# Performance work log

Measured on AMD Instinct MI355X. Metric: run time of the kernel, lower is better.

Reference implementation:

```python
import jax, jax.numpy as jnp
import numpy as np
import math
from jax import lax

K = 3  # kernel size for every layer


def _get_size(h, w, stride, ceil_mode):
    ah, aw = h - (K - 1), w - (K - 1)
    if ceil_mode:
        return math.ceil(ah / stride), math.ceil(aw / stride)
    return ah // stride, aw // stride


def _sample(h, w, stride, ceil_mode, mask_out, rng):
    """Replicates SConv2dAvg.sample: random in-stride offsets per output cell,
    plus bottom-up input mask = union of 3x3 windows of selected positions
    where the downstream mask is active."""
    ah, aw = h - (K - 1), w - (K - 1)
    oh, ow = _get_size(h, w, stride, ceil_mode)
    selh = rng.integers(0, stride, (oh, ow)).astype(np.int32)
    selw = rng.integers(0, stride, (oh, ow)).astype(np.int32)
    resth, restw = oh * stride - ah, ow * stride - aw
    if resth > 0:
        selh[-1, :] = selh[-1, :] % resth
    if restw > 0:
        selw[:, -1] = selw[:, -1] % restw
    ph = selh + (np.arange(oh) * stride)[:, None]  # conv-grid row of selected window
    pw = selw + (np.arange(ow) * stride)[None, :]
    mask_in = np.zeros((h, w), np.int32)
    ys = ph[mask_out == 1]
    xs = pw[mask_out == 1]
    for dy in range(K):
        for dx in range(K):
            mask_in[ys + dy, xs + dx] = 1
    return selh, selw, mask_in


def setup_inputs() -> dict:
    key = jax.random.key(0)
    rng = np.random.default_rng(0)
    B, H0, W0 = 64, 132, 132
    ks = jax.random.split(key, 9)
    x = jax.random.normal(ks[0], (B, 3, H0, W0), jnp.float32)

    def conv_params(kw_, kb_, cout, cin):
        bound = 1.0 / np.sqrt(cin * K * K)
        w = jax.random.uniform(kw_, (cout, cin, K, K), jnp.float32, -bound, bound)
        b = jax.random.uniform(kb_, (cout,), jnp.float32, -bound, bound)
        return w, b

    w1, b1 = conv_params(ks[1], ks[2], 200, 3)
    w2, b2 = conv_params(ks[3], ks[4], 400, 200)
    w3, b3 = conv_params(ks[5], ks[6], 800, 400)
    w4, b4 = conv_params(ks[7], ks[8], 10, 800)

    h1, wd1 = _get_size(H0, W0, 2, False)   # 65,65
    h2, wd2 = _get_size(h1, wd1, 2, False)  # 31,31
    h3, wd3 = _get_size(h2, wd2, 2, True)   # 15,15
    mask3 = np.ones((h3, wd3), np.int32)
    selh3, selw3, mask2 = _sample(h2, wd2, 2, True, mask3, rng)
    selh2, selw2, mask1 = _sample(h1, wd1, 2, False, mask2, rng)
    selh1, selw1, _ = _sample(H0, W0, 2, False, mask1, rng)

    j = jnp.asarray
    return {
        "x": x,
        "w1": w1, "b1": b1, "w2": w2, "b2": b2,
        "w3": w3, "b3": b3, "w4": w4, "b4": b4,
        "selh1": j(selh1), "selw1": j(selw1), "mask1": j(mask1),
        "selh2": j(selh2), "selw2": j(selw2), "mask2": j(mask2),
        "selh3": j(selh3), "selw3": j(selw3), "mask3": j(mask3),
    }


def _sconv_stoch(x, weight, bias, selh, selw, mask, stride):
    """Stochastic strided conv: per output cell, evaluate the 3x3 valid conv at a
    randomly selected position inside its stride x stride block; zero unmasked
    cells (they were never computed), then add bias everywhere."""
    oh, ow = selh.shape
    kh, kw = weight.shape[2], weight.shape[3]
    ph = selh + jnp.arange(oh, dtype=selh.dtype)[:, None] * stride  # (oh,ow)
    pw = selw + jnp.arange(ow, dtype=selw.dtype)[None, :] * stride
    ih = ph[:, :, None, None] + jnp.arange(kh)[None, None, :, None]  # (oh,ow,kh,kw)
    iw = pw[:, :, None, None] + jnp.arange(kw)[None, None, None, :]
    patches = x[:, :, ih, iw]  # (B, Cin, oh, ow, kh, kw)
    out = jnp.einsum('bchwij,ocij->bohw', patches, weight)
    out = jnp.where(mask[None, None] == 1, out, jnp.zeros((), out.dtype))
    return out + bias[None, :, None, None]


def reference(x, w1, b1, w2, b2, w3, b3, w4, b4,
              selh1, selw1, mask1, selh2, selw2, mask2, selh3, selw3, mask3):
    out = jax.nn.relu(_sconv_stoch(x, w1, b1, selh1, selw1, mask1, 2))
    out = jax.nn.relu(_sconv_stoch(out, w2, b2, selh2, selw2, mask2, 2))
    out = jax.nn.relu(_sconv_stoch(out, w3, b3, selh3, selw3, mask3, 2))
    out = lax.conv_general_dilated(out, w4, (1, 1), 'VALID') + b4[None, :, None, None]
    return out.reshape(out.shape[0], -1)
```

## Files before the change

kernel.cpp:

```cpp
#include <hip/hip_runtime.h>
#include <hip/hip_bf16.h>

using bf16 = __hip_bfloat16;
using short8 = __attribute__((ext_vector_type(8))) short;
using sh4 = __attribute__((ext_vector_type(4))) short;
using f32x4 = __attribute__((ext_vector_type(4))) float;

__device__ __align__(16) bf16 g_wp1[16 * 3 * 512];
__device__ __align__(16) bf16 g_wp2[63 * 25 * 512];
__device__ __align__(16) bf16 g_wp3[2 * 117 * 25 * 512];
__device__ __align__(16) bf16 g_wp4[1 * 225 * 512];

__device__ int g_list1[4225];
__device__ int g_list2[961];
__device__ int g_list3[225];
__device__ int g_cnt[3];


__global__ __launch_bounds__(256) void k_pack1(const float* __restrict__ w) {
  int el = blockIdx.x * 256 + threadIdx.x;
  if (el >= 16 * 3 * 512) return;
  int j = el & 7, lane = (el >> 3) & 63, rest = el >> 9;
  int kt = rest % 3, mt = rest / 3;
  int m = mt * 16 + (lane & 15);
  int k = kt * 32 + ((lane >> 4) * 8) + j;
  int chunk = k >> 3, c = k & 7;
  float val = 0.f;
  if (m < 200 && chunk < 9 && c < 3) val = w[((size_t)m * 3 + c) * 9 + chunk];
  g_wp1[el] = __float2bfloat16(val);
}
template <int CIN, int SUBT, int COUT, int KT>
__device__ __forceinline__ void pack_kmaj(const float* __restrict__ w,
                                          bf16* __restrict__ dst, int total) {
  int el = blockIdx.x * 256 + threadIdx.x;
  if (el >= total) return;
  int j = el & 7, lane = (el >> 3) & 63, ti = el >> 9;
  int half = ti / (KT * 25);
  int r2 = ti - half * (KT * 25);
  int kt = r2 / 25, mtl = r2 - kt * 25;
  int mt = half * 25 + mtl;
  int chunk = kt / SUBT, cc = kt - chunk * SUBT;
  int m = mt * 16 + (lane & 15);
  int c = cc * 32 + ((lane >> 4) * 8) + j;
  float val = 0.f;
  if (m < COUT && c < CIN) val = w[((size_t)m * CIN + c) * 9 + chunk];
  dst[el] = __float2bfloat16(val);
}
__global__ __launch_bounds__(256) void k_pack2(const float* __restrict__ w) {
  pack_kmaj<200, 7, 400, 63>(w, g_wp2, 63 * 25 * 512);
}
__global__ __launch_bounds__(256) void k_pack3(const float* __restrict__ w) {
  pack_kmaj<400, 13, 800, 117>(w, g_wp3, 2 * 117 * 25 * 512);
}
__global__ __launch_bounds__(256) void k_pack4(const float* __restrict__ w) {
  int el = blockIdx.x * 256 + threadIdx.x;
  if (el >= 225 * 512) return;
  int j = el & 7, lane = (el >> 3) & 63, rest = el >> 9;
  int kt = rest % 225;
  int chunk = kt / 25, cc = kt - chunk * 25;
  int m = lane & 15;
  int c = cc * 32 + ((lane >> 4) * 8) + j;
  float val = 0.f;
  if (m < 10 && c < 800) val = w[((size_t)m * 800 + c) * 9 + chunk];
  g_wp4[el] = __float2bfloat16(val);
}

__global__ __launch_bounds__(256) void k_compact(const int* __restrict__ m1,
                                                 const int* __restrict__ m2,
                                                 const int* __restrict__ m3) {
  const int which = blockIdx.x;
  const int* m = which == 0 ? m1 : (which == 1 ? m2 : m3);
  int* lst = which == 0 ? g_list1 : (which == 1 ? g_list2 : g_list3);
  const int n = which == 0 ? 4225 : (which == 1 ? 961 : 225);
  const int per = (n + 255) / 256;
  const int lo = threadIdx.x * per;
  const int hi = lo + per < n ? lo + per : n;
  __shared__ int cnt[256];
  __shared__ int off[256];
  int c = 0;
  for (int i = lo; i < hi; ++i) c += (m[i] != 0);
  cnt[threadIdx.x] = c;
  __syncthreads();
  if (threadIdx.x == 0) {
    int s = 0;
    for (int t = 0; t < 256; ++t) { off[t] = s; s += cnt[t]; }
    g_cnt[which] = s;
  }
  __syncthreads();
  int o = off[threadIdx.x];
  for (int i = lo; i < hi; ++i)
    if (m[i] != 0) lst[o++] = i;
}

template <int COUT>
__global__ __launch_bounds__(256) void k_fill_off(const int* __restrict__ mask,
                                                  const float* __restrict__ bias,
                                                  bf16* __restrict__ out_t) {
  constexpr int NFULL = (COUT / 32) * 32;
  constexpr int TW = COUT - NFULL;
  constexpr int TD = TW ? TW * 16 : 1;
  const int pos = blockIdx.x;
  if (mask[pos] != 0) return;
  bf16* base = out_t + (size_t)pos * 64 * COUT;
  for (int idx = threadIdx.x; idx < 64 * COUT / 8; idx += 256) {
    const int e0 = idx * 8;
    int ch0;
    if (e0 < NFULL * 64) {
      const int cc = e0 >> 11;
      const int r = e0 & 2047;
      const int lq = (r >> 7) & 3;
      ch0 = cc * 32 + lq * 8;
    } else {
      const int r = e0 - NFULL * 64;
      const int r2 = r - (r / TD) * TD;
      const int mq = (TW == 16) ? (r2 >> 7) : 0;
      ch0 = NFULL + mq * 8;
    }
    short8 s;
#pragma unroll
    for (int j = 0; j < 8; ++j) {
      float v = bias[ch0 + j];
      v = v > 0.f ? v : 0.f;
      bf16 h = __float2bfloat16(v);
      s[j] = *reinterpret_cast<short*>(&h);
    }
    *reinterpret_cast<short8*>(base + e0) = s;
  }
}

__global__ __launch_bounds__(256) void k_fill_xt(float* __restrict__ p, int n4) {
  int i = blockIdx.x * 256 + threadIdx.x;
  if (i < n4) reinterpret_cast<float4*>(p)[i] = float4{0.f, 0.f, 0.f, 0.f};
}
__global__ __launch_bounds__(256) void k_zero_out(float* __restrict__ p) {
  int i = blockIdx.x * 256 + threadIdx.x;
  if (i < 64 * 10 * 13 * 13) p[i] = 0.f;
}

__global__ __launch_bounds__(256) void k_transpose_x(const float* __restrict__ x,
                                                     bf16* __restrict__ xt) {
  int idx = blockIdx.x * 256 + threadIdx.x;
  constexpr int N = 64 * 3 * 132 * 132;
  if (idx >= N) return;
  int w = idx % 132;
  int t = idx / 132;
  int h = t % 132;
  t /= 132;
  int c = t % 3;
  int b = t / 3;
  xt[((size_t)(h * 132 + w) * 64 + b) * 8 + c] = __float2bfloat16(x[idx]);
}

template <int COUT, int MT>
__device__ __forceinline__ void epilogue_frag(f32x4 (&acc)[MT][4], int pos,
                                              int mt0, int mcnt, int q, int nl,
                                              const float* bias, bf16* out_t) {
  constexpr int NFULL = (COUT / 32) * 32;
  constexpr int TW = COUT - NFULL;
  bf16* cell = out_t + (size_t)pos * (COUT * 64);
#pragma unroll
  for (int ms = 0; ms < MT; ++ms) {
    const int T = mt0 + ms;
    const int mbase = T * 16 + q * 4;
    if (ms < mcnt && mbase < COUT) {
      const float4 bv = *reinterpret_cast<const float4*>(bias + mbase);
#pragma unroll
      for (int t = 0; t < 4; ++t) {
        sh4 s;
#pragma unroll
        for (int r = 0; r < 4; ++r) {
          float vv = acc[ms][t][r] + ((const float*)&bv)[r];
          vv = vv > 0.f ? vv : 0.f;
          bf16 h = __float2bfloat16(vv);
          s[r] = *reinterpret_cast<short*>(&h);
        }
        size_t el;
        if (mbase < NFULL) {
          el = ((size_t)((mbase >> 5) * 4 + t) * 64 +
                (((mbase >> 3) & 3) * 16 + nl)) * 8 + (mbase & 7);
        } else {
          el = (size_t)NFULL * 64 + t * (TW * 16) +
               ((TW == 16) ? (((mbase >> 3) & 1) * 128) : 0) + nl * 8 +
               (mbase & 7);
        }
        *reinterpret_cast<sh4*>(cell + el) = s;
      }
    }
  }
}

template <int CINW, int COUT, int WIN, int OW, int KTILES, int MT>
__device__ __forceinline__ void sconv_body_div(
    const bf16* __restrict__ in_t, const bf16* __restrict__ wp,
    const float* __restrict__ bias, const int* __restrict__ selh,
    const int* __restrict__ selw, const int* __restrict__ list, int which,
    bf16* __restrict__ out_t) {
  const int bid = blockIdx.x;
  if (bid >= g_cnt[which]) return;
  const int pos = list[bid];
  const int tid = threadIdx.x;
  const int lane = tid & 63;
  const int wv = tid >> 6;
  const int nl = lane & 15;
  const int q = lane >> 4;
  const int mt0 = blockIdx.y * (4 * MT) + wv * MT;
  f32x4 acc[MT][4] = {};
  const int y = pos / OW, xq = pos % OW;
  const int ph = selh[pos] + 2 * y;
  const int pw = selw[pos] + 2 * xq;
  const short8* ap = reinterpret_cast<const short8*>(wp);
#pragma unroll
  for (int kt = 0; kt < KTILES; ++kt) {
    int k = kt * 32 + q * 8;
    int chunk = (int)((unsigned)k / (unsigned)CINW);
    int c = k - chunk * CINW;
    if (chunk > 8) { chunk = 8; c = 0; }
    const int di = (chunk * 342) >> 10;
    const int dj = chunk - di * 3;
    const bf16* bp =
        in_t + ((size_t)((ph + di) * WIN + (pw + dj)) * 64 + nl) * CINW + c;
    short8 Bf[4];
#pragma unroll
    for (int t = 0; t < 4; ++t)
      Bf[t] = *reinterpret_cast<const short8*>(bp + (size_t)t * 16 * CINW);
    short8 Af[MT];
#pragma unroll
    for (int ms = 0; ms < MT; ++ms)
      Af[ms] = ap[((size_t)(mt0 + ms) * KTILES + kt) * 64 + lane];
#pragma unroll
    for (int ms = 0; ms < MT; ++ms)
#pragma unroll
      for (int t = 0; t < 4; ++t)
        acc[ms][t] =
            __builtin_amdgcn_mfma_f32_16x16x32_bf16(Af[ms], Bf[t], acc[ms][t], 0, 0, 0);
  }
  epilogue_frag<COUT, MT>(acc, pos, mt0, MT, q, nl, bias, out_t);
}

template <int CIN, int SUBT, int COUT, int WIN, int OW, int NTILE>
__device__ __forceinline__ void sconv_body_pipe(
    const bf16* __restrict__ in_t, const bf16* __restrict__ wp,
    const float* __restrict__ bias, const int* __restrict__ selh,
    const int* __restrict__ selw, const int* __restrict__ list, int which,
    int bid, int myt, bf16* __restrict__ out_t) {
  constexpr int MT = 4;
  constexpr int KTILES = 9 * SUBT;
  constexpr int NFC = CIN / 32;
  constexpr int TIN = CIN - NFC * 32;
  __shared__ __align__(16) bf16 Ab[3][NTILE * 512];
  __shared__ __align__(16) bf16 Bb[3][2 * 2048];
  const int cnt = g_cnt[which];
  if (2 * bid >= cnt) return;
  const int p0 = list[2 * bid];
  const int p1 = list[2 * bid + 1 < cnt ? 2 * bid + 1 : cnt - 1];
  const int tid = threadIdx.x;
  const int lane = tid & 63;
  const int wv = tid >> 6;
  const int g = wv & 7;
  const int pp = wv >> 3;
  const int tstart = (g == 0) ? 0 : 4 + 3 * (g - 1);
  const int tcnt = (g == 0) ? 4 : 3;
  const int stile = (wv < 9) ? wv * 2 : 18 + (wv - 9);
  const int scnt = (wv < 9) ? 2 : 1;
  const int nl = lane & 15;
  const int q = lane >> 4;
  const int y0 = p0 / OW, x0 = p0 % OW;
  const int y1 = p1 / OW, x1 = p1 % OW;
  const int ph0 = selh[p0] + 2 * y0, pw0 = selw[p0] + 2 * x0;
  const int ph1 = selh[p1] + 2 * y1, pw1 = selw[p1] + 2 * x1;

  auto cellp = [&](int ph, int pw, int chunk) -> const bf16* {
    const int di = (chunk * 342) >> 10;
    const int dj = chunk - di * 3;
    return in_t + (size_t)((ph + di) * WIN + (pw + dj)) * (CIN * 64);
  };

  int scc = 0, sch = 0;
  const bf16* scell0 = cellp(ph0, pw0, 0);
  const bf16* scell1 = cellp(ph1, pw1, 0);

  auto stage = [&](int b) {
    const int kt = sch * SUBT + scc;
    const bf16* asrc = wp + ((size_t)kt * NTILE + stile) * 512 + lane * 8;
#pragma unroll
    for (int i = 0; i < 2; ++i) {
      if (i < scnt) {
        __builtin_amdgcn_global_load_lds(
            (const __attribute__((address_space(1))) void*)(asrc + (size_t)i * 512),
            (__attribute__((address_space(3))) void*)(&Ab[b][(stile + i) * 512 +
                                                             lane * 8]),
            16, 0, 0);
      }
    }
    if (wv < 8) {
      const int j = wv & 3;
      const bf16* cell = (wv >> 2) ? scell1 : scell0;
      int boff;
      if (scc < NFC) {
        boff = (scc * 4 + j) * 512;
      } else {
        int jj = (j * 512 < TIN * 64) ? j : 0;
        boff = NFC * 2048 + jj * 512;
      }
      __builtin_amdgcn_global_load_lds(
          (const __attribute__((address_space(1))) void*)(cell + boff + lane * 8),
          (__attribute__((address_space(3))) void*)(&Bb[b][(wv >> 2) * 2048 +
                                                           j * 512 + lane * 8]),
          16, 0, 0);
    }
    if (++scc == SUBT) {
      scc = 0;
      if (++sch > 8) sch = 8;
      scell0 = cellp(ph0, pw0, sch);
      scell1 = cellp(ph1, pw1, sch);
    }
  };

  f32x4 acc[MT][4] = {};

  stage(0);
  stage(1);

  int buf = 0, ccC = 0;
  for (int kt = 0; kt < KTILES; ++kt) {
    __builtin_amdgcn_sched_barrier(0);
    if (kt == KTILES - 1) {
      asm volatile("s_waitcnt vmcnt(0)");
    } else if (wv < 8) {
      asm volatile("s_waitcnt vmcnt(3)");
    } else if (wv == 8) {
      asm volatile("s_waitcnt vmcnt(2)");
    } else {
      asm volatile("s_waitcnt vmcnt(1)");
    }
    __builtin_amdgcn_sched_barrier(0);
    __builtin_amdgcn_s_barrier();
    __builtin_amdgcn_sched_barrier(0);

    short8 Af[MT];
#pragma unroll
    for (int ms = 0; ms < MT; ++ms)
      if (ms < tcnt)
        Af[ms] = *reinterpret_cast<const short8*>(
            &Ab[buf][(tstart + ms) * 512 + lane * 8]);
    short8 Bf[4];
    if (ccC != SUBT - 1) {
#pragma unroll
      for (int t = 0; t < 4; ++t)
        Bf[t] = *reinterpret_cast<const short8*>(
            &Bb[buf][pp * 2048 + t * 512 + lane * 8]);
    } else if (TIN == 8) {
#pragma unroll
      for (int t = 0; t < 4; ++t)
        Bf[t] = *reinterpret_cast<const short8*>(
            &Bb[buf][pp * 2048 + t * 128 + nl * 8]);
    } else {
#pragma unroll
      for (int t = 0; t < 4; ++t)
        Bf[t] = *reinterpret_cast<const short8*>(
            &Bb[buf][pp * 2048 + t * 256 + (q & 1) * 128 + nl * 8]);
    }
    __builtin_amdgcn_s_setprio(1);
#pragma unroll
    for (int ms = 0; ms < MT; ++ms)
      if (ms < tcnt)
#pragma unroll
        for (int t = 0; t < 4; ++t)
          acc[ms][t] = __builtin_amdgcn_mfma_f32_16x16x32_bf16(Af[ms], Bf[t],
                                                               acc[ms][t], 0, 0, 0);
    __builtin_amdgcn_s_setprio(0);
    __builtin_amdgcn_sched_barrier(0);
    if (kt + 2 < KTILES) {
      int sb = buf + 2;
      if (sb >= 3) sb -= 3;
      stage(sb);
    }
    if (++ccC == SUBT) ccC = 0;
    if (++buf == 3) buf = 0;
  }
  const int mt0 = myt * NTILE + tstart;
  epilogue_frag<COUT, MT>(acc, pp ? p1 : p0, mt0, tcnt, q, nl, bias, out_t);
}

__global__ __launch_bounds__(256) void k_sconv1(
    const bf16* __restrict__ in_t, const float* __restrict__ bias,
    const int* __restrict__ selh, const int* __restrict__ selw,
    bf16* __restrict__ out_t) {
  sconv_body_div<8, 200, 132, 65, 3, 4>(in_t, g_wp1, bias, selh, selw, g_list1, 0,
                                        out_t);
}
__global__ __launch_bounds__(1024, 4) void k_sconv2(
    const bf16* __restrict__ in_t, const float* __restrict__ bias,
    const int* __restrict__ selh, const int* __restrict__ selw,
    bf16* __restrict__ out_t) {
  sconv_body_pipe<200, 7, 400, 65, 31, 25>(in_t, g_wp2, bias, selh, selw,
                                           g_list2, 1, blockIdx.x, 0, out_t);
}
__global__ __launch_bounds__(1024, 4) void k_sconv3(
    const bf16* __restrict__ in_t, const float* __restrict__ bias,
    const int* __restrict__ selh, const int* __restrict__ selw,
    bf16* __restrict__ out_t) {
  const int id = blockIdx.x;
  const int xcd = id & 7;
  const int yhalf = xcd >> 2;
  const int slot = (id >> 3) * 4 + (xcd & 3);
  sconv_body_pipe<400, 13, 800, 31, 15, 25>(
      in_t, g_wp3 + (size_t)yhalf * 117 * 25 * 512, bias, selh, selw, g_list3, 2,
      slot, yhalf, out_t);
}

__global__ __launch_bounds__(256) void k_conv4m(
    const bf16* __restrict__ in_t,
    const float* __restrict__ bias,
    float* __restrict__ out) {
  const int pos = blockIdx.x;
  const int y = pos / 13, x = pos % 13;
  const int tid = threadIdx.x;
  const int lane = tid & 63;
  const int wv = tid >> 6;
  const int nl = lane & 15;
  const int q = lane >> 4;
  const int kslice = blockIdx.y * 4 + wv;
  __shared__ f32x4 Racc[4][4][64];
  f32x4 acc[4] = {};
  const short8* ap = reinterpret_cast<const short8*>(g_wp4);
  for (int kt = kslice; kt < 225; kt += 16) {
    const int chunk = kt / 25;
    const int cc = kt - chunk * 25;
    const int di = chunk / 3, dj = chunk - di * 3;
    const bf16* cell = in_t + (size_t)((y + di) * 15 + (x + dj)) * (800 * 64);
    short8 A0 = ap[(size_t)kt * 64 + lane];
    short8 Bf[4];
#pragma unroll
    for (int t = 0; t < 4; ++t)
      Bf[t] = *reinterpret_cast<const short8*>(
          cell + ((size_t)(cc * 4 + t) * 64 + lane) * 8);
#pragma unroll
    for (int t = 0; t < 4; ++t)
      acc[t] = __builtin_amdgcn_mfma_f32_16x16x32_bf16(A0, Bf[t], acc[t], 0, 0, 0);
  }
#pragma unroll
  for (int t = 0; t < 4; ++t) Racc[wv][t][lane] = acc[t];
  __syncthreads();
  if (wv == 0) {
    const int rowb = q * 4;
#pragma unroll
    for (int t = 0; t < 4; ++t) {
      f32x4 s = Racc[0][t][lane];
#pragma unroll
      for (int w2 = 1; w2 < 4; ++w2) {
        f32x4 o = Racc[w2][t][lane];
#pragma unroll
        for (int r = 0; r < 4; ++r) s[r] += o[r];
      }
      const int n = t * 16 + nl;
#pragma unroll
      for (int r = 0; r < 4; ++r) {
        const int m = rowb + r;
        if (m < 10) {
          float v = s[r] + (blockIdx.y == 0 ? bias[m] : 0.f);
          atomicAdd(&out[(((size_t)n * 10 + m) * 13 + y) * 13 + x], v);
        }
      }
    }
  }
}

extern "C" void kernel_launch(void* const* d_in, const int* in_sizes, int n_in,
                              void* d_out, int out_size, void* d_ws, size_t ws_size,
                              hipStream_t stream) {
  const float* x  = (const float*)d_in[0];
  const float* w1 = (const float*)d_in[1];
  const float* b1 = (const float*)d_in[2];
  const float* w2 = (const float*)d_in[3];
  const float* b2 = (const float*)d_in[4];
  const float* w3 = (const float*)d_in[5];
  const float* b3 = (const float*)d_in[6];
  const float* w4 = (const float*)d_in[7];
  const float* b4 = (const float*)d_in[8];
  const int* selh1 = (const int*)d_in[9];
  const int* selw1 = (const int*)d_in[10];
  const int* mask1 = (const int*)d_in[11];
  const int* selh2 = (const int*)d_in[12];
  const int* selw2 = (const int*)d_in[13];
  const int* mask2 = (const int*)d_in[14];
  const int* selh3 = (const int*)d_in[15];
  const int* selw3 = (const int*)d_in[16];
  const int* mask3 = (const int*)d_in[17];

  char* ws = (char*)d_ws;
  bf16* o1t = (bf16*)(ws);
  bf16* xt  = (bf16*)(ws + 108160000);
  bf16* o2t = (bf16*)(ws + 108160000);
  bf16* o3t = (bf16*)(ws);

  k_pack1<<<dim3((16 * 3 * 512 + 255) / 256), dim3(256), 0, stream>>>(w1);
  k_pack2<<<dim3((63 * 25 * 512 + 255) / 256), dim3(256), 0, stream>>>(w2);
  k_pack3<<<dim3((2 * 117 * 25 * 512 + 255) / 256), dim3(256), 0, stream>>>(w3);
  k_pack4<<<dim3((225 * 512 + 255) / 256), dim3(256), 0, stream>>>(w4);
  k_compact<<<dim3(3), dim3(256), 0, stream>>>(mask1, mask2, mask3);
  k_fill_xt<<<dim3((2230272 + 255) / 256), dim3(256), 0, stream>>>((float*)xt, 2230272);
  k_transpose_x<<<dim3((64 * 3 * 132 * 132 + 255) / 256), dim3(256), 0, stream>>>(x, xt);
  k_zero_out<<<dim3((64 * 10 * 13 * 13 + 255) / 256), dim3(256), 0, stream>>>(
      (float*)d_out);

  k_fill_off<200><<<dim3(4225), dim3(256), 0, stream>>>(mask1, b1, o1t);
  k_sconv1<<<dim3(4225, 1), dim3(256), 0, stream>>>(xt, b1, selh1, selw1, o1t);

  k_fill_off<400><<<dim3(961), dim3(256), 0, stream>>>(mask2, b2, o2t);
  k_sconv2<<<dim3(481, 1), dim3(1024), 0, stream>>>(o1t, b2, selh2, selw2, o2t);

  k_fill_off<800><<<dim3(225), dim3(256), 0, stream>>>(mask3, b3, o3t);
  k_sconv3<<<dim3(232, 1), dim3(1024), 0, stream>>>(o2t, b3, selh3, selw3, o3t);

  k_conv4m<<<dim3(13 * 13, 4), dim3(256), 0, stream>>>(o3t, b4, (float*)d_out);
}
```

Measured before the change: 449.2 us.

## Process two k-tiles per barrier with double-buffered LDS staging in pipelined sconv

```diff
diff --git a/kernel.cpp b/kernel.cpp
--- a/kernel.cpp
+++ b/kernel.cpp
@@ -245,10 +245,11 @@
     int bid, int myt, bf16* __restrict__ out_t) {
   constexpr int MT = 4;
   constexpr int KTILES = 9 * SUBT;
+  constexpr int NSTEP = (KTILES + 1) / 2;
   constexpr int NFC = CIN / 32;
   constexpr int TIN = CIN - NFC * 32;
-  __shared__ __align__(16) bf16 Ab[3][NTILE * 512];
-  __shared__ __align__(16) bf16 Bb[3][2 * 2048];
+  __shared__ __align__(16) bf16 Ab[2][2][NTILE * 512];
+  __shared__ __align__(16) bf16 Bb[2][2][2 * 2048];
   const int cnt = g_cnt[which];
   if (2 * bid >= cnt) return;
   const int p0 = list[2 * bid];
@@ -260,8 +261,9 @@
   const int pp = wv >> 3;
   const int tstart = (g == 0) ? 0 : 4 + 3 * (g - 1);
   const int tcnt = (g == 0) ? 4 : 3;
-  const int stile = (wv < 9) ? wv * 2 : 18 + (wv - 9);
-  const int scnt = (wv < 9) ? 2 : 1;
+  const int astart = (wv < 2) ? 4 * wv : 3 * wv + 2;
+  const int acnt = (wv < 2) ? 4 : 3;
+  const int bsub = wv >> 3, bpos = (wv >> 2) & 1, bj = wv & 3;
   const int nl = lane & 15;
   const int q = lane >> 4;
   const int y0 = p0 / OW, x0 = p0 % OW;
@@ -275,108 +277,99 @@
     return in_t + (size_t)((ph + di) * WIN + (pw + dj)) * (CIN * 64);
   };
 
-  int scc = 0, sch = 0;
-  const bf16* scell0 = cellp(ph0, pw0, 0);
-  const bf16* scell1 = cellp(ph1, pw1, 0);
-
-  auto stage = [&](int b) {
-    const int kt = sch * SUBT + scc;
-    const bf16* asrc = wp + ((size_t)kt * NTILE + stile) * 512 + lane * 8;
-#pragma unroll
-    for (int i = 0; i < 2; ++i) {
-      if (i < scnt) {
+  auto stage = [&](int b, int s) {
+#pragma unroll
+    for (int i = 0; i < 4; ++i) {
+      if (i < acnt) {
+        const int T = astart + i;
+        const int sub = (T >= NTILE) ? 1 : 0;
+        const int tl = T - sub * NTILE;
+        int kts = 2 * s + sub;
+        if (kts > KTILES - 1) kts = KTILES - 1;
+        const bf16* asrc = wp + ((size_t)kts * NTILE + tl) * 512 + lane * 8;
         __builtin_amdgcn_global_load_lds(
-            (const __attribute__((address_space(1))) void*)(asrc + (size_t)i * 512),
-            (__attribute__((address_space(3))) void*)(&Ab[b][(stile + i) * 512 +
-                                                             lane * 8]),
+            (const __attribute__((address_space(1))) void*)asrc,
+            (__attribute__((address_space(3))) void*)(&Ab[b][sub][tl * 512 +
+                                                                  lane * 8]),
             16, 0, 0);
       }
     }
-    if (wv < 8) {
-      const int j = wv & 3;
-      const bf16* cell = (wv >> 2) ? scell1 : scell0;
+    {
+      int kts = 2 * s + bsub;
+      if (kts > KTILES - 1) kts = KTILES - 1;
+      const int chunk = kts / SUBT;
+      const int ccs = kts - chunk * SUBT;
+      const bf16* cell = cellp(bpos ? ph1 : ph0, bpos ? pw1 : pw0, chunk);
       int boff;
-      if (scc < NFC) {
-        boff = (scc * 4 + j) * 512;
+      if (ccs < NFC) {
+        boff = (ccs * 4 + bj) * 512;
       } else {
-        int jj = (j * 512 < TIN * 64) ? j : 0;
+        int jj = (bj * 512 < TIN * 64) ? bj : 0;
         boff = NFC * 2048 + jj * 512;
       }
       __builtin_amdgcn_global_load_lds(
           (const __attribute__((address_space(1))) void*)(cell + boff + lane * 8),
-          (__attribute__((address_space(3))) void*)(&Bb[b][(wv >> 2) * 2048 +
-                                                           j * 512 + lane * 8]),
+          (__attribute__((address_space(3))) void*)(&Bb[b][bsub][bpos * 2048 +
+                                                                 bj * 512 +
+                                                                 lane * 8]),
           16, 0, 0);
     }
-    if (++scc == SUBT) {
-      scc = 0;
-      if (++sch > 8) sch = 8;
-      scell0 = cellp(ph0, pw0, sch);
-      scell1 = cellp(ph1, pw1, sch);
-    }
   };
 
   f32x4 acc[MT][4] = {};
 
-  stage(0);
-  stage(1);
-
-  int buf = 0, ccC = 0;
-  for (int kt = 0; kt < KTILES; ++kt) {
+  stage(0, 0);
+
+  for (int s = 0; s < NSTEP; ++s) {
+    const int cur = s & 1;
     __builtin_amdgcn_sched_barrier(0);
-    if (kt == KTILES - 1) {
-      asm volatile("s_waitcnt vmcnt(0)");
-    } else if (wv < 8) {
-      asm volatile("s_waitcnt vmcnt(3)");
-    } else if (wv == 8) {
-      asm volatile("s_waitcnt vmcnt(2)");
-    } else {
-      asm volatile("s_waitcnt vmcnt(1)");
-    }
+    asm volatile("s_waitcnt vmcnt(0)");
     __builtin_amdgcn_sched_barrier(0);
     __builtin_amdgcn_s_barrier();
     __builtin_amdgcn_sched_barrier(0);
-
-    short8 Af[MT];
-#pragma unroll
-    for (int ms = 0; ms < MT; ++ms)
-      if (ms < tcnt)
-        Af[ms] = *reinterpret_cast<const short8*>(
-            &Ab[buf][(tstart + ms) * 512 + lane * 8]);
-    short8 Bf[4];
-    if (ccC != SUBT - 1) {
-#pragma unroll
-      for (int t = 0; t < 4; ++t)
-        Bf[t] = *reinterpret_cast<const short8*>(
-            &Bb[buf][pp * 2048 + t * 512 + lane * 8]);
-    } else if (TIN == 8) {
-#pragma unroll
-      for (int t = 0; t < 4; ++t)
-        Bf[t] = *reinterpret_cast<const short8*>(
-            &Bb[buf][pp * 2048 + t * 128 + nl * 8]);
-    } else {
-#pragma unroll
-      for (int t = 0; t < 4; ++t)
-        Bf[t] = *reinterpret_cast<const short8*>(
-            &Bb[buf][pp * 2048 + t * 256 + (q & 1) * 128 + nl * 8]);
-    }
-    __builtin_amdgcn_s_setprio(1);
-#pragma unroll
-    for (int ms = 0; ms < MT; ++ms)
-      if (ms < tcnt)
-#pragma unroll
-        for (int t = 0; t < 4; ++t)
-          acc[ms][t] = __builtin_amdgcn_mfma_f32_16x16x32_bf16(Af[ms], Bf[t],
-                                                               acc[ms][t], 0, 0, 0);
-    __builtin_amdgcn_s_setprio(0);
+    if (s + 1 < NSTEP) stage(cur ^ 1, s + 1);
     __builtin_amdgcn_sched_barrier(0);
-    if (kt + 2 < KTILES) {
-      int sb = buf + 2;
-      if (sb >= 3) sb -= 3;
-      stage(sb);
-    }
-    if (++ccC == SUBT) ccC = 0;
-    if (++buf == 3) buf = 0;
+
+#pragma unroll
+    for (int sub = 0; sub < 2; ++sub) {
+      const int kts = 2 * s + sub;
+      if (kts < KTILES) {
+        const int chunk = kts / SUBT;
+        const int ccs = kts - chunk * SUBT;
+        short8 Af[MT];
+#pragma unroll
+        for (int ms = 0; ms < MT; ++ms)
+          if (ms < tcnt)
+            Af[ms] = *reinterpret_cast<const short8*>(
+                &Ab[cur][sub][(tstart + ms) * 512 + lane * 8]);
+        short8 Bf[4];
+        if (ccs != SUBT - 1) {
+#pragma unroll
+          for (int t = 0; t < 4; ++t)
+            Bf[t] = *reinterpret_cast<const short8*>(
+                &Bb[cur][sub][pp * 2048 + t * 512 + lane * 8]);
+        } else if (TIN == 8) {
+#pragma unroll
+          for (int t = 0; t < 4; ++t)
+            Bf[t] = *reinterpret_cast<const short8*>(
+                &Bb[cur][sub][pp * 2048 + t * 128 + nl * 8]);
+        } else {
+#pragma unroll
+          for (int t = 0; t < 4; ++t)
+            Bf[t] = *reinterpret_cast<const short8*>(
+                &Bb[cur][sub][pp * 2048 + t * 256 + (q & 1) * 128 + nl * 8]);
+        }
+        __builtin_amdgcn_s_setprio(1);
+#pragma unroll
+        for (int ms = 0; ms < MT; ++ms)
+          if (ms < tcnt)
+#pragma unroll
+            for (int t = 0; t < 4; ++t)
+              acc[ms][t] = __builtin_amdgcn_mfma_f32_16x16x32_bf16(
+                  Af[ms], Bf[t], acc[ms][t], 0, 0, 0);
+        __builtin_amdgcn_s_setprio(0);
+      }
+    }
   }
   const int mt0 = myt * NTILE + tstart;
   epilogue_frag<COUT, MT>(acc, pp ? p1 : p0, mt0, tcnt, q, nl, bias, out_t);
```

New measurement: 465.6 us. 3.6% more time.
